# Optimization experiments

Measured on AMD Instinct MI355X. Metric: run time of the kernel, lower is better.

## Reference

```python
import jax, jax.numpy as jnp
import numpy as np

N, K, D = 131072, 2048, 1024
EPS = 1e-12  # matches torch F.normalize default eps


def setup_inputs() -> dict:
    key = jax.random.key(0)
    k1, k2 = jax.random.split(key)
    vectors = jax.random.normal(k1, (N, D), dtype=jnp.float32)
    # centroids are L2-normalized once at construction time (init-time .data normalize)
    c = jax.random.normal(k2, (K, D), dtype=jnp.float32)
    centroids = c / jnp.maximum(jnp.linalg.norm(c, axis=1, keepdims=True), EPS)
    return {"vectors": vectors, "centroids": centroids}


def reference(vectors, centroids):
    # F.normalize(vectors, p=2, dim=1): divide by clamped L2 norm
    norms = jnp.maximum(jnp.linalg.norm(vectors, axis=1, keepdims=True), EPS)
    vectors_norm = vectors / norms
    # cosine similarity against (already-normalized-at-init) centroids: [N, K]
    similarity = jnp.einsum('nd,kd->nk', vectors_norm, centroids)
    # hard assignment: top-1 over clusters
    assignments = jnp.argmax(similarity, axis=1)
    return assignments
```

## Files before the change

### kernel.cpp

```cpp
#include <hip/hip_runtime.h>
#include <stdint.h>
#include <math.h>

#define N_ROWS 131072
#define K_CEN  2048
#define D_DIM  1024
#define BM     64
#define TAU    0.02f
#define CAND_CAP 64

typedef short bf16x8 __attribute__((ext_vector_type(8)));
typedef float f32x4  __attribute__((ext_vector_type(4)));

__device__ __forceinline__ unsigned short f2bf(float f) {
  unsigned u = __float_as_uint(f);
  return (unsigned short)((u + 0x7fffu + ((u >> 16) & 1u)) >> 16);
}
__device__ __forceinline__ unsigned f2ord(float f) {
  unsigned u = __float_as_uint(f);
  return (u & 0x80000000u) ? ~u : (u | 0x80000000u);
}
__device__ __forceinline__ float ord2f(unsigned o) {
  unsigned u = (o & 0x80000000u) ? (o & 0x7fffffffu) : ~o;
  return __uint_as_float(u);
}

__global__ __launch_bounds__(256) void cvt_centroids(const float* __restrict__ cen,
                                                     unsigned short* __restrict__ outb) {
  int i = blockIdx.x * 256 + threadIdx.x;
  float4 v = reinterpret_cast<const float4*>(cen)[i];
  ushort4 r;
  r.x = f2bf(v.x); r.y = f2bf(v.y); r.z = f2bf(v.z); r.w = f2bf(v.w);
  reinterpret_cast<ushort4*>(outb)[i] = r;
}

__global__ __launch_bounds__(512, 1) void assign_rows(
    const float* __restrict__ vec, const float* __restrict__ cenf,
    const unsigned short* __restrict__ cenb, int* __restrict__ out)
{
  __shared__ unsigned short v_lds[BM * D_DIM];
  __shared__ unsigned rowmax_ord[BM];
  __shared__ int cand_cnt[BM];
  __shared__ unsigned candv[BM][CAND_CAP];
  __shared__ unsigned short candc[BM][CAND_CAP];

  const int tid  = threadIdx.x;
  const int lane = tid & 63;
  const int wid  = tid >> 6;
  const long row0 = (long)blockIdx.x * BM;

  for (int r = tid; r < BM; r += 512) { rowmax_ord[r] = f2ord(-3.0e38f); cand_cnt[r] = 0; }

  #pragma unroll
  for (int it = 0; it < 16; ++it) {
    int cid = it * 512 + tid;
    int r  = cid >> 7;
    int dc = (cid & 127) << 3;
    const f32x4* vp = reinterpret_cast<const f32x4*>(vec + (row0 + r) * D_DIM + dc);
    f32x4 a = __builtin_nontemporal_load(vp);
    f32x4 b = __builtin_nontemporal_load(vp + 1);
    bf16x8 pk;
    pk[0]=(short)f2bf(a[0]); pk[1]=(short)f2bf(a[1]); pk[2]=(short)f2bf(a[2]); pk[3]=(short)f2bf(a[3]);
    pk[4]=(short)f2bf(b[0]); pk[5]=(short)f2bf(b[1]); pk[6]=(short)f2bf(b[2]); pk[7]=(short)f2bf(b[3]);
    int byt = (r << 11) + (dc << 1);
    *reinterpret_cast<bf16x8*>(reinterpret_cast<char*>(v_lds) + (byt ^ ((r & 7) << 4))) = pk;
  }
  __syncthreads();

  const int l15 = lane & 15;
  const int lq  = lane >> 4;
  const int amask = (l15 & 7) << 4;
  const int abase = (l15 << 11) + (lq << 4);
  const char* v_bytes = reinterpret_cast<const char*>(v_lds);
  const char* c_bytes = reinterpret_cast<const char*>(cenb);

  for (int cb = 0; cb < 4; ++cb) {
    const int colbase = (wid << 8) + (cb << 6);
    const size_t bbase = ((size_t)(colbase + l15) << 11) + (size_t)(lq << 4);
    const char* bp0 = c_bytes + bbase;
    const char* bp1 = bp0 + 32768;
    const char* bp2 = bp1 + 32768;
    const char* bp3 = bp2 + 32768;

    f32x4 acc[4][4];
    #pragma unroll
    for (int mi = 0; mi < 4; ++mi)
      #pragma unroll
      for (int ni = 0; ni < 4; ++ni) acc[mi][ni] = (f32x4){0.f,0.f,0.f,0.f};

    bf16x8 breg[2][4];
    bf16x8 areg[2][4];

    breg[0][0] = *reinterpret_cast<const bf16x8*>(bp0);
    breg[0][1] = *reinterpret_cast<const bf16x8*>(bp1);
    breg[0][2] = *reinterpret_cast<const bf16x8*>(bp2);
    breg[0][3] = *reinterpret_cast<const bf16x8*>(bp3);
    breg[1][0] = *reinterpret_cast<const bf16x8*>(bp0 + 64);
    breg[1][1] = *reinterpret_cast<const bf16x8*>(bp1 + 64);
    breg[1][2] = *reinterpret_cast<const bf16x8*>(bp2 + 64);
    breg[1][3] = *reinterpret_cast<const bf16x8*>(bp3 + 64);
    {
      int ta = abase ^ amask;
      #pragma unroll
      for (int mi = 0; mi < 4; ++mi)
        areg[0][mi] = *reinterpret_cast<const bf16x8*>(v_bytes + ta + (mi << 15));
    }
    __builtin_amdgcn_sched_barrier(0);

    #pragma unroll
    for (int kc = 0; kc < 32; ++kc) {
      if (kc + 1 < 32) {
        int ta = (abase + ((kc + 1) << 6)) ^ amask;
        #pragma unroll
        for (int mi = 0; mi < 4; ++mi)
          areg[(kc + 1) & 1][mi] = *reinterpret_cast<const bf16x8*>(v_bytes + ta + (mi << 15));
      }
      __builtin_amdgcn_sched_barrier(0);
      __builtin_amdgcn_s_setprio(1);
      #pragma unroll
      for (int ni = 0; ni < 4; ++ni) {
        #pragma unroll
        for (int mi = 0; mi < 4; ++mi)
          acc[mi][ni] = __builtin_amdgcn_mfma_f32_16x16x32_bf16(areg[kc & 1][mi], breg[kc & 1][ni], acc[mi][ni], 0, 0, 0);
        if (kc + 2 < 32) {
          const int ko = (kc + 2) << 6;
          const char* bp = ni==0?bp0: ni==1?bp1: ni==2?bp2: bp3;
          breg[kc & 1][ni] = *reinterpret_cast<const bf16x8*>(bp + ko);
        }
      }
      __builtin_amdgcn_s_setprio(0);
      __builtin_amdgcn_sched_barrier(0);
    }

    #pragma unroll
    for (int mi = 0; mi < 4; ++mi) {
      #pragma unroll
      for (int j = 0; j < 4; ++j) {
        float mv = fmaxf(fmaxf(acc[mi][0][j], acc[mi][1][j]),
                         fmaxf(acc[mi][2][j], acc[mi][3][j]));
        mv = fmaxf(mv, __shfl_xor(mv, 1));
        mv = fmaxf(mv, __shfl_xor(mv, 2));
        mv = fmaxf(mv, __shfl_xor(mv, 4));
        mv = fmaxf(mv, __shfl_xor(mv, 8));
        if (l15 == 0) {
          int row = (mi << 4) + (lq << 2) + j;
          atomicMax(&rowmax_ord[row], f2ord(mv));
        }
      }
    }
    #pragma unroll
    for (int mi = 0; mi < 4; ++mi) {
      #pragma unroll
      for (int j = 0; j < 4; ++j) {
        int row = (mi << 4) + (lq << 2) + j;
        float thr = ord2f(rowmax_ord[row]) - TAU;
        #pragma unroll
        for (int ni = 0; ni < 4; ++ni) {
          float v = acc[mi][ni][j];
          if (v >= thr) {
            int slot = atomicAdd(&cand_cnt[row], 1);
            if (slot < CAND_CAP) {
              candv[row][slot] = f2ord(v);
              candc[row][slot] = (unsigned short)(colbase + (ni << 4) + l15);
            }
          }
        }
      }
    }
  }
  __syncthreads();

  for (int r = wid; r < BM; r += 8) {
    const long grow = row0 + r;
    int cnt = cand_cnt[r]; cnt = cnt > CAND_CAP ? CAND_CAP : cnt;
    const unsigned thro = f2ord(ord2f(rowmax_ord[r]) - TAU);

    bool sv = (lane < cnt) && (candv[r][lane] >= thro);
    unsigned long long bal = __ballot(sv);
    int nsurv = __popcll(bal);
    if (nsurv == 1) {
      int idx = __builtin_ctzll(bal);
      if (lane == 0) out[grow] = (int)candc[r][idx];
      continue;
    }
    const bool use_filter = (nsurv >= 1);

    const float* vrow = vec + grow * D_DIM + (lane << 4);
    float va[16];
    #pragma unroll
    for (int i = 0; i < 16; ++i) va[i] = vrow[i];
    double bestv = -1.0e300;
    int    besti = 0x7fffffff;
    for (int ci = 0; ci < cnt; ++ci) {
      if (use_filter && candv[r][ci] < thro) continue;
      const int col = (int)candc[r][ci];
      const float* crow = cenf + ((size_t)col << 10) + (lane << 4);
      double s = 0.0;
      #pragma unroll
      for (int i = 0; i < 16; ++i) s = fma((double)va[i], (double)crow[i], s);
      s += __shfl_xor(s, 32);
      s += __shfl_xor(s, 16);
      s += __shfl_xor(s, 8);
      s += __shfl_xor(s, 4);
      s += __shfl_xor(s, 2);
      s += __shfl_xor(s, 1);
      if (s > bestv || (s == bestv && col < besti)) { bestv = s; besti = col; }
    }
    if (lane == 0) out[grow] = besti;
  }
}

extern "C" void kernel_launch(void* const* d_in, const int* in_sizes, int n_in,
                              void* d_out, int out_size, void* d_ws, size_t ws_size,
                              hipStream_t stream) {
  const float* vec  = (const float*)d_in[0];
  const float* cenf = (const float*)d_in[1];
  unsigned short* cenb = (unsigned short*)d_ws;
  int* out = (int*)d_out;

  cvt_centroids<<<(K_CEN * D_DIM / 4) / 256, 256, 0, stream>>>(cenf, cenb);
  assign_rows<<<N_ROWS / BM, 512, 0, stream>>>(vec, cenf, cenb, out);
}
```

Before: 1.081 ms.

## Switch candidate GEMM from bf16 to fp8 MFMA with exact-rescoring fallback

New measurement: 2.683 ms. 148% more time.

```diff
diff --git a/kernel.cpp b/kernel.cpp
--- a/kernel.cpp
+++ b/kernel.cpp
@@ -6,16 +6,13 @@
 #define K_CEN  2048
 #define D_DIM  1024
 #define BM     64
-#define TAU    0.02f
-#define CAND_CAP 64
-
-typedef short bf16x8 __attribute__((ext_vector_type(8)));
+#define CSCALE 16.0f
+#define TAUS   6.5f
+#define CAND_CAP 32
+
 typedef float f32x4  __attribute__((ext_vector_type(4)));
-
-__device__ __forceinline__ unsigned short f2bf(float f) {
-  unsigned u = __float_as_uint(f);
-  return (unsigned short)((u + 0x7fffu + ((u >> 16) & 1u)) >> 16);
-}
+typedef int   i32x4  __attribute__((ext_vector_type(4)));
+
 __device__ __forceinline__ unsigned f2ord(float f) {
   unsigned u = __float_as_uint(f);
   return (u & 0x80000000u) ? ~u : (u | 0x80000000u);
@@ -24,21 +21,25 @@
   unsigned u = (o & 0x80000000u) ? (o & 0x7fffffffu) : ~o;
   return __uint_as_float(u);
 }
+__device__ __forceinline__ unsigned pk4_fp8(float a0, float a1, float a2, float a3) {
+  unsigned w = 0;
+  w = __builtin_amdgcn_cvt_pk_fp8_f32(a0, a1, w, false);
+  w = __builtin_amdgcn_cvt_pk_fp8_f32(a2, a3, w, true);
+  return w;
+}
 
 __global__ __launch_bounds__(256) void cvt_centroids(const float* __restrict__ cen,
-                                                     unsigned short* __restrict__ outb) {
+                                                     unsigned* __restrict__ outb) {
   int i = blockIdx.x * 256 + threadIdx.x;
   float4 v = reinterpret_cast<const float4*>(cen)[i];
-  ushort4 r;
-  r.x = f2bf(v.x); r.y = f2bf(v.y); r.z = f2bf(v.z); r.w = f2bf(v.w);
-  reinterpret_cast<ushort4*>(outb)[i] = r;
+  outb[i] = pk4_fp8(v.x * CSCALE, v.y * CSCALE, v.z * CSCALE, v.w * CSCALE);
 }
 
 __global__ __launch_bounds__(512, 1) void assign_rows(
     const float* __restrict__ vec, const float* __restrict__ cenf,
-    const unsigned short* __restrict__ cenb, int* __restrict__ out)
+    const unsigned char* __restrict__ cenb, int* __restrict__ out)
 {
-  __shared__ unsigned short v_lds[BM * D_DIM];
+  __shared__ unsigned char v_lds[BM * D_DIM];
   __shared__ unsigned rowmax_ord[BM];
   __shared__ int cand_cnt[BM];
   __shared__ unsigned candv[BM][CAND_CAP];
@@ -49,38 +50,42 @@
   const int wid  = tid >> 6;
   const long row0 = (long)blockIdx.x * BM;
 
-  for (int r = tid; r < BM; r += 512) { rowmax_ord[r] = f2ord(-3.0e38f); cand_cnt[r] = 0; }
+  if (tid < BM) { rowmax_ord[tid] = f2ord(-3.0e38f); cand_cnt[tid] = 0; }
 
   #pragma unroll
-  for (int it = 0; it < 16; ++it) {
+  for (int it = 0; it < 8; ++it) {
     int cid = it * 512 + tid;
-    int r  = cid >> 7;
-    int dc = (cid & 127) << 3;
+    int r  = cid >> 6;
+    int dc = (cid & 63) << 4;
     const f32x4* vp = reinterpret_cast<const f32x4*>(vec + (row0 + r) * D_DIM + dc);
     f32x4 a = __builtin_nontemporal_load(vp);
     f32x4 b = __builtin_nontemporal_load(vp + 1);
-    bf16x8 pk;
-    pk[0]=(short)f2bf(a[0]); pk[1]=(short)f2bf(a[1]); pk[2]=(short)f2bf(a[2]); pk[3]=(short)f2bf(a[3]);
-    pk[4]=(short)f2bf(b[0]); pk[5]=(short)f2bf(b[1]); pk[6]=(short)f2bf(b[2]); pk[7]=(short)f2bf(b[3]);
-    int byt = (r << 11) + (dc << 1);
-    *reinterpret_cast<bf16x8*>(reinterpret_cast<char*>(v_lds) + (byt ^ ((r & 7) << 4))) = pk;
+    f32x4 c = __builtin_nontemporal_load(vp + 2);
+    f32x4 d = __builtin_nontemporal_load(vp + 3);
+    i32x4 pk;
+    pk[0] = (int)pk4_fp8(a[0], a[1], a[2], a[3]);
+    pk[1] = (int)pk4_fp8(b[0], b[1], b[2], b[3]);
+    pk[2] = (int)pk4_fp8(c[0], c[1], c[2], c[3]);
+    pk[3] = (int)pk4_fp8(d[0], d[1], d[2], d[3]);
+    int byt = (r << 10) + dc;
+    *reinterpret_cast<i32x4*>(reinterpret_cast<char*>(v_lds) + (byt ^ ((r & 7) << 4))) = pk;
   }
   __syncthreads();
 
   const int l15 = lane & 15;
   const int lq  = lane >> 4;
   const int amask = (l15 & 7) << 4;
-  const int abase = (l15 << 11) + (lq << 4);
+  const int abase = (l15 << 10) + (lq << 3);
   const char* v_bytes = reinterpret_cast<const char*>(v_lds);
   const char* c_bytes = reinterpret_cast<const char*>(cenb);
 
   for (int cb = 0; cb < 4; ++cb) {
     const int colbase = (wid << 8) + (cb << 6);
-    const size_t bbase = ((size_t)(colbase + l15) << 11) + (size_t)(lq << 4);
+    const size_t bbase = ((size_t)(colbase + l15) << 10) + (size_t)(lq << 3);
     const char* bp0 = c_bytes + bbase;
-    const char* bp1 = bp0 + 32768;
-    const char* bp2 = bp1 + 32768;
-    const char* bp3 = bp2 + 32768;
+    const char* bp1 = bp0 + 16384;
+    const char* bp2 = bp1 + 16384;
+    const char* bp3 = bp2 + 16384;
 
     f32x4 acc[4][4];
     #pragma unroll
@@ -88,32 +93,31 @@
       #pragma unroll
       for (int ni = 0; ni < 4; ++ni) acc[mi][ni] = (f32x4){0.f,0.f,0.f,0.f};
 
-    bf16x8 breg[2][4];
-    bf16x8 areg[2][4];
-
-    breg[0][0] = *reinterpret_cast<const bf16x8*>(bp0);
-    breg[0][1] = *reinterpret_cast<const bf16x8*>(bp1);
-    breg[0][2] = *reinterpret_cast<const bf16x8*>(bp2);
-    breg[0][3] = *reinterpret_cast<const bf16x8*>(bp3);
-    breg[1][0] = *reinterpret_cast<const bf16x8*>(bp0 + 64);
-    breg[1][1] = *reinterpret_cast<const bf16x8*>(bp1 + 64);
-    breg[1][2] = *reinterpret_cast<const bf16x8*>(bp2 + 64);
-    breg[1][3] = *reinterpret_cast<const bf16x8*>(bp3 + 64);
+    long breg[3][4];
+    long areg[2][4];
+
+    #pragma unroll
+    for (int k = 0; k < 3; ++k) {
+      breg[k][0] = *reinterpret_cast<const long*>(bp0 + (k << 5));
+      breg[k][1] = *reinterpret_cast<const long*>(bp1 + (k << 5));
+      breg[k][2] = *reinterpret_cast<const long*>(bp2 + (k << 5));
+      breg[k][3] = *reinterpret_cast<const long*>(bp3 + (k << 5));
+    }
     {
       int ta = abase ^ amask;
       #pragma unroll
       for (int mi = 0; mi < 4; ++mi)
-        areg[0][mi] = *reinterpret_cast<const bf16x8*>(v_bytes + ta + (mi << 15));
+        areg[0][mi] = *reinterpret_cast<const long*>(v_bytes + ta + (mi << 14));
     }
     __builtin_amdgcn_sched_barrier(0);
 
     #pragma unroll
     for (int kc = 0; kc < 32; ++kc) {
       if (kc + 1 < 32) {
-        int ta = (abase + ((kc + 1) << 6)) ^ amask;
+        int ta = (abase + ((kc + 1) << 5)) ^ amask;
         #pragma unroll
         for (int mi = 0; mi < 4; ++mi)
-          areg[(kc + 1) & 1][mi] = *reinterpret_cast<const bf16x8*>(v_bytes + ta + (mi << 15));
+          areg[(kc + 1) & 1][mi] = *reinterpret_cast<const long*>(v_bytes + ta + (mi << 14));
       }
       __builtin_amdgcn_sched_barrier(0);
       __builtin_amdgcn_s_setprio(1);
@@ -121,11 +125,12 @@
       for (int ni = 0; ni < 4; ++ni) {
         #pragma unroll
         for (int mi = 0; mi < 4; ++mi)
-          acc[mi][ni] = __builtin_amdgcn_mfma_f32_16x16x32_bf16(areg[kc & 1][mi], breg[kc & 1][ni], acc[mi][ni], 0, 0, 0);
-        if (kc + 2 < 32) {
-          const int ko = (kc + 2) << 6;
+          acc[mi][ni] = __builtin_amdgcn_mfma_f32_16x16x32_fp8_fp8(
+              areg[kc & 1][mi], breg[kc % 3][ni], acc[mi][ni], 0, 0, 0);
+        if (kc + 3 < 32) {
+          const int ko = (kc + 3) << 5;
           const char* bp = ni==0?bp0: ni==1?bp1: ni==2?bp2: bp3;
-          breg[kc & 1][ni] = *reinterpret_cast<const bf16x8*>(bp + ko);
+          breg[kc % 3][ni] = *reinterpret_cast<const long*>(bp + ko);
         }
       }
       __builtin_amdgcn_s_setprio(0);
@@ -148,12 +153,13 @@
         }
       }
     }
+    __syncthreads();
     #pragma unroll
     for (int mi = 0; mi < 4; ++mi) {
       #pragma unroll
       for (int j = 0; j < 4; ++j) {
         int row = (mi << 4) + (lq << 2) + j;
-        float thr = ord2f(rowmax_ord[row]) - TAU;
+        float thr = ord2f(rowmax_ord[row]) - TAUS;
         #pragma unroll
         for (int ni = 0; ni < 4; ++ni) {
           float v = acc[mi][ni][j];
@@ -172,41 +178,61 @@
 
   for (int r = wid; r < BM; r += 8) {
     const long grow = row0 + r;
-    int cnt = cand_cnt[r]; cnt = cnt > CAND_CAP ? CAND_CAP : cnt;
-    const unsigned thro = f2ord(ord2f(rowmax_ord[r]) - TAU);
-
-    bool sv = (lane < cnt) && (candv[r][lane] >= thro);
-    unsigned long long bal = __ballot(sv);
-    int nsurv = __popcll(bal);
-    if (nsurv == 1) {
-      int idx = __builtin_ctzll(bal);
-      if (lane == 0) out[grow] = (int)candc[r][idx];
-      continue;
-    }
-    const bool use_filter = (nsurv >= 1);
-
+    const int raw = cand_cnt[r];
     const float* vrow = vec + grow * D_DIM + (lane << 4);
-    float va[16];
-    #pragma unroll
-    for (int i = 0; i < 16; ++i) va[i] = vrow[i];
-    double bestv = -1.0e300;
-    int    besti = 0x7fffffff;
-    for (int ci = 0; ci < cnt; ++ci) {
-      if (use_filter && candv[r][ci] < thro) continue;
-      const int col = (int)candc[r][ci];
-      const float* crow = cenf + ((size_t)col << 10) + (lane << 4);
-      double s = 0.0;
-      #pragma unroll
-      for (int i = 0; i < 16; ++i) s = fma((double)va[i], (double)crow[i], s);
-      s += __shfl_xor(s, 32);
-      s += __shfl_xor(s, 16);
-      s += __shfl_xor(s, 8);
-      s += __shfl_xor(s, 4);
-      s += __shfl_xor(s, 2);
-      s += __shfl_xor(s, 1);
-      if (s > bestv || (s == bestv && col < besti)) { bestv = s; besti = col; }
-    }
-    if (lane == 0) out[grow] = besti;
+
+    if (raw <= CAND_CAP) {
+      const unsigned thro = f2ord(ord2f(rowmax_ord[r]) - TAUS);
+      bool sv = (lane < raw) && (candv[r][lane] >= thro);
+      unsigned long long bal = __ballot(sv);
+      int nsurv = __popcll(bal);
+      if (nsurv == 1) {
+        int idx = __builtin_ctzll(bal);
+        if (lane == 0) out[grow] = (int)candc[r][idx];
+        continue;
+      }
+      float va[16];
+      #pragma unroll
+      for (int i = 0; i < 16; ++i) va[i] = vrow[i];
+      double bestv = -1.0e300;
+      int    besti = 0x7fffffff;
+      for (int ci = 0; ci < raw; ++ci) {
+        if (candv[r][ci] < thro) continue;
+        const int col = (int)candc[r][ci];
+        const float* crow = cenf + ((size_t)col << 10) + (lane << 4);
+        double s = 0.0;
+        #pragma unroll
+        for (int i = 0; i < 16; ++i) s = fma((double)va[i], (double)crow[i], s);
+        s += __shfl_xor(s, 32);
+        s += __shfl_xor(s, 16);
+        s += __shfl_xor(s, 8);
+        s += __shfl_xor(s, 4);
+        s += __shfl_xor(s, 2);
+        s += __shfl_xor(s, 1);
+        if (s > bestv || (s == bestv && col < besti)) { bestv = s; besti = col; }
+      }
+      if (lane == 0) out[grow] = besti;
+    } else {
+      float va[16];
+      #pragma unroll
+      for (int i = 0; i < 16; ++i) va[i] = vrow[i];
+      double bestv = -1.0e300;
+      int    besti = 0x7fffffff;
+      for (int col = 0; col < K_CEN; ++col) {
+        const float* crow = cenf + ((size_t)col << 10) + (lane << 4);
+        double s = 0.0;
+        #pragma unroll
+        for (int i = 0; i < 16; ++i) s = fma((double)va[i], (double)crow[i], s);
+        s += __shfl_xor(s, 32);
+        s += __shfl_xor(s, 16);
+        s += __shfl_xor(s, 8);
+        s += __shfl_xor(s, 4);
+        s += __shfl_xor(s, 2);
+        s += __shfl_xor(s, 1);
+        if (s > bestv) { bestv = s; besti = col; }
+      }
+      if (lane == 0) out[grow] = besti;
+    }
   }
 }
 
@@ -215,9 +241,10 @@
                               hipStream_t stream) {
   const float* vec  = (const float*)d_in[0];
   const float* cenf = (const float*)d_in[1];
-  unsigned short* cenb = (unsigned short*)d_ws;
+  unsigned* cenb = (unsigned*)d_ws;
   int* out = (int*)d_out;
 
   cvt_centroids<<<(K_CEN * D_DIM / 4) / 256, 256, 0, stream>>>(cenf, cenb);
-  assign_rows<<<N_ROWS / BM, 512, 0, stream>>>(vec, cenf, cenb, out);
-}
+  assign_rows<<<N_ROWS / BM, 512, 0, stream>>>(vec, cenf,
+                                               (const unsigned char*)cenb, out);
+}
```
